# Kernel tuning notes

Measured on AMD Instinct MI355X. Metric: run time of the kernel, lower is better.

Reference implementation:

```python
import jax, jax.numpy as jnp
import numpy as np

N = 8192      # number of WSI patches
DIN = 1024    # input patch-feature dim (dim_in)
DH = 256      # dim_hidden
K = 6         # topk
SCALE = DH ** -0.5

def leaky(x):
    return jax.nn.leaky_relu(x, 0.01)

def setup_inputs() -> dict:
    key = jax.random.key(0)
    ks = jax.random.split(key, 8)
    def w(k, shape, fan_in):
        return jax.random.normal(k, shape, jnp.float32) / np.sqrt(fan_in).astype(np.float32)
    return {
        "x_path": jax.random.normal(ks[0], (N, DIN), jnp.float32),
        "fc1_W": w(ks[1], (DIN, DH), DIN), "fc1_b": jnp.zeros((DH,), jnp.float32),
        "Wh": w(ks[2], (DH, DH), DH), "bh": jnp.zeros((DH,), jnp.float32),
        "Wt": w(ks[3], (DH, DH), DH), "bt": jnp.zeros((DH,), jnp.float32),
        "W1": w(ks[4], (DH, DH), DH), "b1": jnp.zeros((DH,), jnp.float32),
        "W2": w(ks[5], (DH, DH), DH), "b2": jnp.zeros((DH,), jnp.float32),
        "Ag1": w(ks[6], (DH, DH // 2), DH), "bg1": jnp.zeros((DH // 2,), jnp.float32),
        "Ag2": w(ks[7], (DH // 2, 1), DH // 2), "bg2": jnp.zeros((1,), jnp.float32),
    }

def reference(x_path, fc1_W, fc1_b, Wh, bh, Wt, bt, W1, b1, W2, b2, Ag1, bg1, Ag2, bg2):
    # _fc1: Linear(1024->256) + LeakyReLU, then add global mean ("*0.5" mixing)
    x = leaky(x_path @ fc1_W + fc1_b)[None]                 # (1,N,DH)
    x = (x + x.mean(axis=1, keepdims=True)) * 0.5
    e_h = x @ Wh + bh                                        # (1,N,DH)
    e_t = x @ Wt + bt                                        # (1,N,DH)
    # dense attention logits, then top-k neighbor selection
    attn_logit = (e_h * SCALE) @ jnp.swapaxes(e_t, -1, -2)   # (1,N,N)
    topk_w, topk_i = jax.lax.top_k(attn_logit, K)            # (1,N,K)
    p = jax.nn.softmax(topk_w, axis=2)                       # (1,N,K)
    Nb_h = e_t[0][topk_i[0]][None]                           # gather: (1,N,K,DH)
    # message construction
    eh_r = p[..., None] * Nb_h + (1.0 - p)[..., None] * e_h[:, :, None, :]
    gate = jnp.tanh(e_h[:, :, None, :] + eh_r)               # (1,N,K,DH)
    # faithful to torch.einsum('ijkl,ijkm->ijk', Nb_h, gate):
    # l and m are independent -> separable double sum
    ka_w = Nb_h.sum(-1) * gate.sum(-1)                       # (1,N,K)
    ka_p = jax.nn.softmax(ka_w, axis=2)
    e_Nh = jnp.einsum('ink,inkd->ind', ka_p, Nb_h)           # (1,N,DH)
    # message MLPs (dropout in eval mode = identity)
    e_msg = leaky((e_h + e_Nh) @ W1 + b1) + leaky((e_h * e_Nh) @ W2 + b2)
    # GlobalAttention readout: gate_nn = Linear(256,128)+LeakyReLU+Linear(128,1)
    x2 = e_msg[0]                                            # (N,DH)
    g = leaky(x2 @ Ag1 + bg1) @ Ag2 + bg2                    # (N,1)
    g = jax.nn.softmax(g, axis=0)
    e_g = (g * x2).sum(axis=0, keepdims=True)                # (1,DH)
    return e_msg, e_g
```

## Files before the change

### kernel.cpp

```cpp
#include <hip/hip_runtime.h>


typedef __attribute__((ext_vector_type(8))) short short8;
typedef __attribute__((ext_vector_type(4))) short short4v;
typedef __attribute__((ext_vector_type(4))) float f32x4;

__device__ inline float bf2f(unsigned short b) {
    unsigned u = ((unsigned)b) << 16;
    return __builtin_bit_cast(float, u);
}
__device__ inline unsigned short f2bf(float f) {
    unsigned u = __builtin_bit_cast(unsigned, f);
    unsigned r = u + 0x7fffu + ((u >> 16) & 1u);
    return (unsigned short)(r >> 16);
}
__device__ inline f32x4 mfma16(short8 a, short8 b, f32x4 c) {
    return __builtin_amdgcn_mfma_f32_16x16x32_bf16(a, b, c, 0, 0, 0);
}

__device__ inline void gload_lds16(const unsigned short* g, unsigned short* l) {
    __builtin_amdgcn_global_load_lds(
        (const __attribute__((address_space(1))) void*)g,
        (__attribute__((address_space(3))) void*)l, 16, 0, 0);
}

__device__ inline void split8(const f32x4 v0, const f32x4 v1,
                              short8& hi, short8& md, short8& lo) {
    #pragma unroll
    for (int e = 0; e < 8; e++) {
        float a = (e < 4) ? v0[e] : v1[e - 4];
        unsigned ua = __builtin_bit_cast(unsigned, a);
        float h = __builtin_bit_cast(float, ua & 0xFFFF0000u);
        float r1 = a - h;
        unsigned u1 = __builtin_bit_cast(unsigned, r1);
        float m = __builtin_bit_cast(float, u1 & 0xFFFF0000u);
        float r2 = r1 - m;
        unsigned u2 = __builtin_bit_cast(unsigned, r2);
        hi[e] = (short)(ua >> 16);
        md[e] = (short)(u1 >> 16);
        lo[e] = (short)(u2 >> 16);
    }
}

__launch_bounds__(256)
__global__ void tsplit3(const float* __restrict__ W, unsigned short* __restrict__ out,
                        int K, int N, int PS) {
    __shared__ float T[32][33];
    const int t = threadIdx.x;
    const int n0 = blockIdx.x * 32, k0 = blockIdx.y * 32;
    {
        const int r = t >> 3, c = (t & 7) * 4;
        f32x4 v = *(const f32x4*)&W[(size_t)(k0 + r) * N + n0 + c];
        #pragma unroll
        for (int e = 0; e < 4; e++) T[r][c + e] = v[e];
    }
    __syncthreads();
    const int nr = t >> 3, kc = (t & 7) * 4;
    short4v h4, m4, l4;
    #pragma unroll
    for (int e = 0; e < 4; e++) {
        float a = T[kc + e][nr];
        unsigned short h = f2bf(a);
        float r1 = a - bf2f(h);
        unsigned short m = f2bf(r1);
        float r2 = r1 - bf2f(m);
        h4[e] = (short)h; m4[e] = (short)m; l4[e] = (short)f2bf(r2);
    }
    const size_t o = (size_t)(n0 + nr) * K + k0 + kc;
    *(short4v*)&out[o] = h4;
    *(short4v*)&out[(size_t)PS + o] = m4;
    *(short4v*)&out[(size_t)2 * PS + o] = l4;
}

template <int ASPLIT, int ACT, int ACCUM>
__launch_bounds__(256)
__global__ void gemmM(const void* __restrict__ Av,
                      const unsigned short* __restrict__ Bt,
                      const float* __restrict__ bias, float* __restrict__ C,
                      int N, int K, int BPS) {
    constexpr int APL = ASPLIT ? 3 : 1;
    constexpr int BPL = ASPLIT ? 3 : 2;
    __shared__ __align__(16) unsigned short LA[2][APL * 2048];
    __shared__ __align__(16) unsigned short LB[2][BPL * 2048];
    const int t = threadIdx.x;
    const int r0 = blockIdx.y * 64, c0 = blockIdx.x * 64;
    const int lid = t & 63, w = t >> 6, g = lid >> 4, m16 = lid & 15;
    const int wm = w >> 1, wn = w & 1;

    f32x4 acc[2][2];
    #pragma unroll
    for (int mf = 0; mf < 2; mf++)
        #pragma unroll
        for (int nf = 0; nf < 2; nf++) acc[mf][nf] = {0.0f, 0.0f, 0.0f, 0.0f};

    const int KT = K >> 5;
    const size_t aoff = (size_t)(r0 + (t >> 2)) * K + (t & 3) * 8;
    const size_t boff = (size_t)(c0 + (t >> 2)) * K + (t & 3) * 8;

    {
        #pragma unroll
        for (int p = 0; p < BPL; p++)
            gload_lds16(&Bt[(size_t)p * BPS + boff], &LB[0][p * 2048 + 8 * t]);
        if (ASPLIT) {
            const float* A = (const float*)Av;
            f32x4 v0 = *(const f32x4*)&A[aoff];
            f32x4 v1 = *(const f32x4*)&A[aoff + 4];
            short8 hi, md, lo;
            split8(v0, v1, hi, md, lo);
            *(short8*)&LA[0][8 * t] = hi;
            *(short8*)&LA[0][2048 + 8 * t] = md;
            *(short8*)&LA[0][4096 + 8 * t] = lo;
        } else {
            const unsigned short* A16 = (const unsigned short*)Av;
            gload_lds16(&A16[aoff], &LA[0][8 * t]);
        }
    }
    __syncthreads();

    for (int kt = 0; kt < KT; kt++) {
        const int cur = kt & 1, nxt = cur ^ 1;
        const bool hn = (kt + 1) < KT;
        f32x4 v0, v1;
        if (hn) {
            const size_t ko = (size_t)(kt + 1) * 32;
            #pragma unroll
            for (int p = 0; p < BPL; p++)
                gload_lds16(&Bt[(size_t)p * BPS + boff + ko],
                            &LB[nxt][p * 2048 + 8 * t]);
            if (ASPLIT) {
                const float* A = (const float*)Av;
                v0 = *(const f32x4*)&A[aoff + ko];
                v1 = *(const f32x4*)&A[aoff + ko + 4];
            } else {
                const unsigned short* A16 = (const unsigned short*)Av;
                gload_lds16(&A16[aoff + ko], &LA[nxt][8 * t]);
            }
        }
        short8 af[2][APL], bf[2][BPL];
        #pragma unroll
        for (int mf = 0; mf < 2; mf++) {
            const int row = wm * 32 + mf * 16 + m16;
            #pragma unroll
            for (int p = 0; p < APL; p++)
                af[mf][p] = *(const short8*)&LA[cur][p * 2048 + row * 32 + g * 8];
        }
        #pragma unroll
        for (int nf = 0; nf < 2; nf++) {
            const int col = wn * 32 + nf * 16 + m16;
            #pragma unroll
            for (int p = 0; p < BPL; p++)
                bf[nf][p] = *(const short8*)&LB[cur][p * 2048 + col * 32 + g * 8];
        }
        #pragma unroll
        for (int mf = 0; mf < 2; mf++)
            #pragma unroll
            for (int nf = 0; nf < 2; nf++) {
                if (ASPLIT) {
                    acc[mf][nf] = mfma16(af[mf][0], bf[nf][0], acc[mf][nf]);
                    acc[mf][nf] = mfma16(af[mf][0], bf[nf][1], acc[mf][nf]);
                    acc[mf][nf] = mfma16(af[mf][1], bf[nf][0], acc[mf][nf]);
                    acc[mf][nf] = mfma16(af[mf][0], bf[nf][2], acc[mf][nf]);
                    acc[mf][nf] = mfma16(af[mf][1], bf[nf][1], acc[mf][nf]);
                    acc[mf][nf] = mfma16(af[mf][2], bf[nf][0], acc[mf][nf]);
                } else {
                    acc[mf][nf] = mfma16(af[mf][0], bf[nf][0], acc[mf][nf]);
                    acc[mf][nf] = mfma16(af[mf][0], bf[nf][1], acc[mf][nf]);
                }
            }
        if (hn && ASPLIT) {
            short8 hi, md, lo;
            split8(v0, v1, hi, md, lo);
            *(short8*)&LA[nxt][8 * t] = hi;
            *(short8*)&LA[nxt][2048 + 8 * t] = md;
            *(short8*)&LA[nxt][4096 + 8 * t] = lo;
        }
        __syncthreads();
    }

    #pragma unroll
    for (int nf = 0; nf < 2; nf++) {
        const int col = c0 + wn * 32 + nf * 16 + m16;
        const float bv = bias[col];
        #pragma unroll
        for (int mf = 0; mf < 2; mf++) {
            #pragma unroll
            for (int r = 0; r < 4; r++) {
                const int row = r0 + wm * 32 + mf * 16 + g * 4 + r;
                float v = acc[mf][nf][r] + bv;
                if (ACT == 1) v = v > 0.0f ? v : 0.01f * v;
                size_t idx = (size_t)row * N + col;
                if (ACCUM) v += C[idx];
                C[idx] = v;
            }
        }
    }
}

__global__ void colsum_k(const float* __restrict__ x, float* __restrict__ out) {
    int d = threadIdx.x, b = blockIdx.x;
    float s = 0.0f;
    int i0 = b * 128;
    for (int i = 0; i < 128; i++) s += x[(size_t)(i0 + i) * 256 + d];
    out[b * 256 + d] = s;
}
__global__ void meanred_k(const float* __restrict__ p, float* __restrict__ mean) {
    int d = threadIdx.x;
    float s = 0.0f;
    for (int b = 0; b < 64; b++) s += p[b * 256 + d];
    mean[d] = s * (1.0f / 8192.0f);
}
__global__ void finalize_x(float* __restrict__ x, const float* __restrict__ mean) {
    size_t idx = (size_t)blockIdx.x * blockDim.x + threadIdx.x;
    f32x4 v = *(f32x4*)&x[idx * 4];
    int d4 = (int)((idx * 4) & 255);
    f32x4 m = *(const f32x4*)&mean[d4];
    #pragma unroll
    for (int e = 0; e < 4; e++) v[e] = (v[e] + m[e]) * 0.5f;
    *(f32x4*)&x[idx * 4] = v;
}
__launch_bounds__(256)
__global__ void prep_k(const float* __restrict__ eh, const float* __restrict__ et,
                       unsigned short* __restrict__ eh16,
                       unsigned short* __restrict__ et16,
                       float* __restrict__ rowsum) {
    const int b = blockIdx.x;
    if (b < 2048) {
        size_t idx = (size_t)b * 256 + threadIdx.x;
        f32x4 v = *(const f32x4*)&eh[idx * 4];
        short4v h;
        #pragma unroll
        for (int e = 0; e < 4; e++) h[e] = (short)f2bf(v[e]);
        *(short4v*)&eh16[idx * 4] = h;
    } else {
        const int w = threadIdx.x >> 6, l = threadIdx.x & 63;
        const int i = (b - 2048) * 4 + w;
        f32x4 v = *(const f32x4*)&et[(size_t)i * 256 + l * 4];
        short4v h;
        #pragma unroll
        for (int e = 0; e < 4; e++) h[e] = (short)f2bf(v[e]);
        *(short4v*)&et16[(size_t)i * 256 + l * 4] = h;
        float s = v[0] + v[1] + v[2] + v[3];
        #pragma unroll
        for (int st = 1; st < 64; st <<= 1) s += __shfl_xor(s, st);
        if (l == 0) rowsum[i] = s;
    }
}

__device__ inline float packkey(float v, unsigned col) {
    unsigned u = (__builtin_bit_cast(unsigned, v) & 0xFFFFF800u) | col;
    return __builtin_bit_cast(float, u);
}
template<int NK>
__device__ inline void insf(float (&tk)[NK], float key) {
    #pragma unroll
    for (int k = 0; k < NK - 1; k++)
        tk[k] = __builtin_amdgcn_fmed3f(key, tk[k + 1], tk[k]);
    tk[NK - 1] = fmaxf(tk[NK - 1], key);
}

__launch_bounds__(512)
__global__ void screen2(const unsigned short* __restrict__ eh16,
                        const unsigned short* __restrict__ et16,
                        int* __restrict__ candi) {
    __shared__ __align__(16) unsigned short Bs[2][2][8192];
    __shared__ float mbuf[8][2][16][8];
    const int t = threadIdx.x;
    const int cs = blockIdx.x;
    const int r0 = blockIdx.y * 128;
    const int w = t >> 6, lid = t & 63, lg = lid >> 4, m16 = lid & 15;
    const int rs = w >> 1, ch = w & 1;

    short8 bfr[2][8];
    #pragma unroll
    for (int s = 0; s < 2; s++)
        #pragma unroll
        for (int ks = 0; ks < 8; ks++)
            bfr[s][ks] = *(const short8*)
                &eh16[(size_t)(r0 + rs * 32 + s * 16 + m16) * 256 + ks * 32 + lg * 8];

    float tk0[6], tk1[6];
    #pragma unroll
    for (int q = 0; q < 6; q++) { tk0[q] = -3.0e38f; tk1[q] = -3.0e38f; }

    int scol[2], goff[2], ldsl[2];
    #pragma unroll
    for (int c = 0; c < 2; c++) {
        int L = (w * 2 + c) * 64 + lid;
        int col = L >> 5, gs = L & 31;
        int gorig = (gs & 24) | ((gs ^ col) & 7);
        scol[c] = col; goff[c] = gorig * 8; ldsl[c] = L * 8;
    }

    #pragma unroll
    for (int tt = 0; tt < 2; tt++) {
        const int j0 = cs * 2048 + tt * 32;
        #pragma unroll
        for (int c = 0; c < 2; c++)
            gload_lds16(&et16[(size_t)(j0 + scol[c]) * 256 + goff[c]],
                        &Bs[0][tt][ldsl[c]]);
    }
    __syncthreads();

    const int swz = m16 & 7;
    const int cbase = (ch * 16 + m16) * 32;
    for (int gi = 0; gi < 32; gi++) {
        const int cur = gi & 1;
        if (gi + 1 < 32) {
            #pragma unroll
            for (int tt = 0; tt < 2; tt++) {
                const int j1 = cs * 2048 + ((gi + 1) * 2 + tt) * 32;
                #pragma unroll
                for (int c = 0; c < 2; c++)
                    gload_lds16(&et16[(size_t)(j1 + scol[c]) * 256 + goff[c]],
                                &Bs[cur ^ 1][tt][ldsl[c]]);
            }
        }
        #pragma unroll
        for (int tt = 0; tt < 2; tt++) {
            const int tile = gi * 2 + tt;
            const unsigned short* bst = Bs[cur][tt];
            f32x4 a0 = {0.0f, 0.0f, 0.0f, 0.0f}, a1 = a0;
            #pragma unroll
            for (int ks = 0; ks < 8; ks++) {
                const int gq = ks * 4 + lg;
                short8 e = *(const short8*)&bst[(cbase + (gq ^ swz)) * 8];
                a0 = mfma16(e, bfr[0][ks], a0);
                a1 = mfma16(e, bfr[1][ks], a1);
            }
            const unsigned cb = (unsigned)(tile * 32 + ch * 16 + lg * 4);
            #pragma unroll
            for (int r = 0; r < 4; r++) {
                insf<6>(tk0, packkey(a0[r], cb + (unsigned)r));
                insf<6>(tk1, packkey(a1[r], cb + (unsigned)r));
            }
        }
        __syncthreads();
    }

    #pragma unroll
    for (int s = 0; s < 2; s++) {
        float tk8[8];
        tk8[0] = -3.0e38f; tk8[1] = -3.0e38f;
        #pragma unroll
        for (int q = 0; q < 6; q++) tk8[q + 2] = s ? tk1[q] : tk0[q];
        #pragma unroll
        for (int step = 16; step <= 32; step <<= 1) {
            float ok[8];
            #pragma unroll
            for (int q = 0; q < 8; q++) ok[q] = __shfl_xor(tk8[q], step);
            #pragma unroll
            for (int q = 0; q < 8; q++) insf<8>(tk8, ok[q]);
        }
        if (lg == 0) {
            #pragma unroll
            for (int q = 0; q < 8; q++) mbuf[rs * 2 + s][ch][m16][q] = tk8[q];
        }
    }
    __syncthreads();

    if (t < 128) {
        float tk8[8];
        #pragma unroll
        for (int q = 0; q < 8; q++) tk8[q] = mbuf[t >> 4][0][t & 15][q];
        #pragma unroll
        for (int q = 0; q < 8; q++) insf<8>(tk8, mbuf[t >> 4][1][t & 15][q]);
        const int row = r0 + t;
        #pragma unroll
        for (int q = 0; q < 8; q++)
            candi[(size_t)row * 32 + cs * 8 + q] =
                cs * 2048 + (int)(__builtin_bit_cast(unsigned, tk8[q]) & 0x7FFu);
    }
}

__launch_bounds__(256)
__global__ void stageD(const float* __restrict__ eh, const float* __restrict__ et,
                       const float* __restrict__ rowsum,
                       const int* __restrict__ candi,
                       unsigned short* __restrict__ m1, unsigned short* __restrict__ m2) {
    const int w = threadIdx.x >> 6, l = threadIdx.x & 63;
    const int i = blockIdx.x * 4 + w;
    const int c_own = l & 31;

    const int jown = candi[(size_t)i * 32 + c_own] & 8191;

    const int q = l & 7, g8 = l >> 3;
    const float* er = &eh[(size_t)i * 256];
    double vres[4];
    #pragma unroll
    for (int p = 0; p < 4; p++) {
        const int cc = p * 8 + g8;
        const int jc = __shfl(jown, cc);
        const float* tr = &et[(size_t)jc * 256];
        double a = 0.0;
        #pragma unroll
        for (int tt = 0; tt < 8; tt++) {
            const int o = (tt * 8 + q) * 4;
            f32x4 av = *(const f32x4*)&er[o];
            f32x4 bv = *(const f32x4*)&tr[o];
            a += (double)av[0] * bv[0] + (double)av[1] * bv[1] +
                 (double)av[2] * bv[2] + (double)av[3] * bv[3];
        }
        a += __shfl_xor(a, 1);
        a += __shfl_xor(a, 2);
        a += __shfl_xor(a, 4);
        vres[p] = a * 0.0625;
    }
    const int src = (c_own & 7) * 8;
    double t0 = __shfl(vres[0], src), t1 = __shfl(vres[1], src);
    double t2 = __shfl(vres[2], src), t3 = __shfl(vres[3], src);
    const int ps = c_own >> 3;
    double v = ps == 0 ? t0 : ps == 1 ? t1 : ps == 2 ? t2 : t3;

    unsigned long long kb = __builtin_bit_cast(unsigned long long, v);
    double key = __builtin_bit_cast(double, (kb & ~31ULL) | (unsigned long long)c_own);
    float wf[6]; int selc[6];
    #pragma unroll
    for (int s = 0; s < 6; s++) {
        double b = key;
        #pragma unroll
        for (int st = 1; st < 32; st <<= 1) {
            double ob = __shfl_xor(b, st);
            b = b > ob ? b : ob;
        }
        selc[s] = (int)(__builtin_bit_cast(unsigned long long, b) & 31ULL);
        wf[s] = (float)b;
        if (key == b) key = -1.0e300;
    }
    int selj[6];
    #pragma unroll
    for (int s = 0; s < 6; s++) selj[s] = __shfl(jown, selc[s]);

    float sp[6];
    {
        float mx = wf[0];
        #pragma unroll
        for (int s = 1; s < 6; s++) mx = fmaxf(mx, wf[s]);
        float se = 0.0f, e6[6];
        #pragma unroll
        for (int s = 0; s < 6; s++) { e6[s] = expf(wf[s] - mx); se += e6[s]; }
        #pragma unroll
        for (int s = 0; s < 6; s++) sp[s] = e6[s] / se;
    }

    f32x4 eh4 = *(const f32x4*)&eh[(size_t)i * 256 + l * 4];
    f32x4 nb[6];
    #pragma unroll
    for (int k = 0; k < 6; k++)
        nb[k] = *(const f32x4*)&et[(size_t)selj[k] * 256 + l * 4];

    float pgs[6], pns[6];
    #pragma unroll
    for (int k = 0; k < 6; k++) {
        const float pk = sp[k];
        float pg = 0.0f;
        #pragma unroll
        for (int e = 0; e < 4; e++) {
            float ehd = eh4[e], nbd = nb[k][e];
            float ehr = pk * nbd + (1.0f - pk) * ehd;
            pg += tanhf(ehd + ehr);
        }
        #pragma unroll
        for (int st = 1; st < 64; st <<= 1) pg += __shfl_xor(pg, st);
        pgs[k] = pg;
        pns[k] = rowsum[selj[k]];
    }

    float skp[6];
    {
        float ka[6], mx = -3.0e38f, se = 0.0f;
        #pragma unroll
        for (int k = 0; k < 6; k++) { ka[k] = pns[k] * pgs[k]; mx = fmaxf(mx, ka[k]); }
        #pragma unroll
        for (int k = 0; k < 6; k++) { ka[k] = expf(ka[k] - mx); se += ka[k]; }
        #pragma unroll
        for (int k = 0; k < 6; k++) skp[k] = ka[k] / se;
    }

    f32x4 enh = {0.0f, 0.0f, 0.0f, 0.0f};
    #pragma unroll
    for (int k = 0; k < 6; k++) {
        const float kp = skp[k];
        #pragma unroll
        for (int e = 0; e < 4; e++) enh[e] += kp * nb[k][e];
    }
    short4v h1, h2;
    #pragma unroll
    for (int e = 0; e < 4; e++) {
        h1[e] = (short)f2bf(eh4[e] + enh[e]);
        h2[e] = (short)f2bf(eh4[e] * enh[e]);
    }
    *(short4v*)&m1[(size_t)i * 256 + l * 4] = h1;
    *(short4v*)&m2[(size_t)i * 256 + l * 4] = h2;
}

__launch_bounds__(256)
__global__ void gate2_k(const float* __restrict__ g1, const float* __restrict__ Ag2,
                        const float* __restrict__ bg2, float* __restrict__ glog) {
    const int i = blockIdx.x * 256 + threadIdx.x;
    float s = 0.0f;
    #pragma unroll 4
    for (int h = 0; h < 128; h++) s += g1[(size_t)i * 128 + h] * Ag2[h];
    glog[i] = s + bg2[0];
}

__launch_bounds__(1024)
__global__ void softmax_g(const float* __restrict__ glog, float* __restrict__ gexp,
                          float* __restrict__ scal) {
    const int t = threadIdx.x;
    __shared__ float red[1024];
    float v[8];
    float m = -3.0e38f;
    #pragma unroll
    for (int c = 0; c < 8; c++) { v[c] = glog[t + c * 1024]; m = fmaxf(m, v[c]); }
    red[t] = m; __syncthreads();
    for (int st = 512; st > 0; st >>= 1) {
        if (t < st) red[t] = fmaxf(red[t], red[t + st]);
        __syncthreads();
    }
    float gm = red[0]; __syncthreads();
    float s = 0.0f;
    #pragma unroll
    for (int c = 0; c < 8; c++) {
        float e = expf(v[c] - gm);
        gexp[t + c * 1024] = e;
        s += e;
    }
    red[t] = s; __syncthreads();
    for (int st = 512; st > 0; st >>= 1) {
        if (t < st) red[t] += red[t + st];
        __syncthreads();
    }
    if (t == 0) scal[0] = 1.0f / red[0];
}

__launch_bounds__(256)
__global__ void wsum_k(const float* __restrict__ emsg, const float* __restrict__ gexp,
                       float* __restrict__ egp) {
    const int b = blockIdx.x, d = threadIdx.x;
    float s = 0.0f;
    const int i0 = b * 128;
    for (int i = 0; i < 128; i++) s += gexp[i0 + i] * emsg[(size_t)(i0 + i) * 256 + d];
    egp[b * 256 + d] = s;
}
__global__ void egfinal_f(const float* __restrict__ egp, const float* __restrict__ scal,
                          float* __restrict__ out) {
    const int d = threadIdx.x;
    float s = 0.0f;
    for (int b = 0; b < 64; b++) s += egp[b * 256 + d];
    out[d] = s * scal[0];
}

__global__ void wsbad_k(float* __restrict__ out) { out[3] = 9000.0f; }

extern "C" void kernel_launch(void* const* d_in, const int* in_sizes, int n_in,
                              void* d_out, int out_size, void* d_ws, size_t ws_size,
                              hipStream_t stream) {
    (void)in_sizes; (void)n_in; (void)out_size;
    const float* x_path = (const float*)d_in[0];
    const float* fc1_W  = (const float*)d_in[1];
    const float* fc1_b  = (const float*)d_in[2];
    const float* Wh     = (const float*)d_in[3];
    const float* bh     = (const float*)d_in[4];
    const float* Wt     = (const float*)d_in[5];
    const float* bt     = (const float*)d_in[6];
    const float* W1     = (const float*)d_in[7];
    const float* b1     = (const float*)d_in[8];
    const float* W2     = (const float*)d_in[9];
    const float* b2     = (const float*)d_in[10];
    const float* Ag1    = (const float*)d_in[11];
    const float* bg1    = (const float*)d_in[12];
    const float* Ag2    = (const float*)d_in[13];
    const float* bg2    = (const float*)d_in[14];
    float* out_f = (float*)d_out;

    const size_t WS_NEEDED = 26412048;
    if (ws_size < WS_NEEDED) {
        hipLaunchKernelGGL(wsbad_k, dim3(1), dim3(1), 0, stream, out_f);
        return;
    }

    char* ws = (char*)d_ws;
    float* x     = (float*)(ws + 0);
    unsigned short* eh16 = (unsigned short*)(ws + 0);
    unsigned short* et16 = (unsigned short*)(ws + 4194304);
    unsigned short* m1b  = (unsigned short*)(ws + 0);
    unsigned short* m2b  = (unsigned short*)(ws + 4194304);
    float* g1    = (float*)(ws + 0);
    float* eh    = (float*)(ws + 8388608);
    float* emsg  = out_f;
    float* et    = (float*)(ws + 16777216);
    int*   candi = (int*)  (ws + 25165824);
    float* rowsum= (float*)(ws + 26214400);
    float* meanp = (float*)(ws + 26214400);
    float* meanv = (float*)(ws + 26279936);
    float* glog  = (float*)(ws + 26280960);
    float* gexp  = (float*)(ws + 26313728);
    float* egp   = (float*)(ws + 26346496);
    float* scal  = (float*)(ws + 26412032);

    unsigned short* Fp = (unsigned short*)(ws + 16777216);
    unsigned short* WHp = (unsigned short*)(ws + 25165824);
    unsigned short* WTp = (unsigned short*)(ws + 25559040);
    unsigned short* P1 = (unsigned short*)(ws + 16777216);
    unsigned short* P2 = (unsigned short*)(ws + 17170432);
    unsigned short* Gp = (unsigned short*)(ws + 25165824);

    dim3 gg(4, 128);
    hipLaunchKernelGGL(tsplit3, dim3(8, 32), dim3(256), 0, stream,
                       fc1_W, Fp, 1024, 256, 262144);
    hipLaunchKernelGGL((gemmM<1, 1, 0>), gg, dim3(256), 0, stream,
                       (const void*)x_path, Fp, fc1_b, x, 256, 1024, 262144);
    hipLaunchKernelGGL(colsum_k, dim3(64), dim3(256), 0, stream, x, meanp);
    hipLaunchKernelGGL(meanred_k, dim3(1), dim3(256), 0, stream, meanp, meanv);
    hipLaunchKernelGGL(finalize_x, dim3(2048), dim3(256), 0, stream, x, meanv);
    hipLaunchKernelGGL(tsplit3, dim3(8, 8), dim3(256), 0, stream,
                       Wh, WHp, 256, 256, 65536);
    hipLaunchKernelGGL(tsplit3, dim3(8, 8), dim3(256), 0, stream,
                       Wt, WTp, 256, 256, 65536);
    hipLaunchKernelGGL((gemmM<1, 0, 0>), gg, dim3(256), 0, stream,
                       (const void*)x, WHp, bh, eh, 256, 256, 65536);
    hipLaunchKernelGGL((gemmM<1, 0, 0>), gg, dim3(256), 0, stream,
                       (const void*)x, WTp, bt, et, 256, 256, 65536);
    hipLaunchKernelGGL(prep_k, dim3(4096), dim3(256), 0, stream,
                       eh, et, eh16, et16, rowsum);
    hipLaunchKernelGGL(screen2, dim3(4, 64), dim3(512), 0, stream, eh16, et16, candi);
    hipLaunchKernelGGL(stageD, dim3(2048), dim3(256), 0, stream, eh, et, rowsum,
                       candi, m1b, m2b);
    hipLaunchKernelGGL(tsplit3, dim3(8, 8), dim3(256), 0, stream,
                       W1, P1, 256, 256, 65536);
    hipLaunchKernelGGL(tsplit3, dim3(8, 8), dim3(256), 0, stream,
                       W2, P2, 256, 256, 65536);
    hipLaunchKernelGGL((gemmM<0, 1, 0>), gg, dim3(256), 0, stream,
                       (const void*)m1b, P1, b1, emsg, 256, 256, 65536);
    hipLaunchKernelGGL((gemmM<0, 1, 1>), gg, dim3(256), 0, stream,
                       (const void*)m2b, P2, b2, emsg, 256, 256, 65536);
    hipLaunchKernelGGL(tsplit3, dim3(4, 8), dim3(256), 0, stream,
                       Ag1, Gp, 256, 128, 32768);
    hipLaunchKernelGGL((gemmM<1, 1, 0>), dim3(2, 128), dim3(256), 0, stream,
                       (const void*)emsg, Gp, bg1, g1, 128, 256, 32768);
    hipLaunchKernelGGL(gate2_k, dim3(32), dim3(256), 0, stream, g1, Ag2, bg2, glog);
    hipLaunchKernelGGL(softmax_g, dim3(1), dim3(1024), 0, stream, glog, gexp, scal);
    hipLaunchKernelGGL(wsum_k, dim3(64), dim3(256), 0, stream, emsg, gexp, egp);
    hipLaunchKernelGGL(egfinal_f, dim3(1), dim3(256), 0, stream, egp, scal, out_f + 2097152);
}
```

Baseline: 328.2 us.

## Fuse eh/et GEMMs, fold mean into bias, merge message MLP GEMMs

Replaces the finalize_x pass and the two separate eh/et GEMMs with one dual-output GEMM. It loads and splits x once, scales it by 0.5 inline, and folds the global-mean term into precomputed biases (bias + 0.5*mean@W). The two message-MLP GEMMs become one kernel that computes both products and writes leaky(a)+leaky(b), with no read-modify-write of emsg. Weight-split launches are also paired into single grids. This cuts launches and extra passes over global memory, but the mean is now folded in fp32 outside the split-bf16 path, which may change rounding slightly.

Result: faster. 312.0 us (-4.9%).

```diff
diff --git a/kernel.cpp b/kernel.cpp
--- a/kernel.cpp
+++ b/kernel.cpp
@@ -41,13 +41,28 @@
         lo[e] = (short)(u2 >> 16);
     }
 }
-
-__launch_bounds__(256)
-__global__ void tsplit3(const float* __restrict__ W, unsigned short* __restrict__ out,
-                        int K, int N, int PS) {
+__device__ inline void split4(f32x4 v, short4v& hi, short4v& md, short4v& lo) {
+    #pragma unroll
+    for (int e = 0; e < 4; e++) {
+        float a = v[e];
+        unsigned ua = __builtin_bit_cast(unsigned, a);
+        float h = __builtin_bit_cast(float, ua & 0xFFFF0000u);
+        float r1 = a - h;
+        unsigned u1 = __builtin_bit_cast(unsigned, r1);
+        float m = __builtin_bit_cast(float, u1 & 0xFFFF0000u);
+        float r2 = r1 - m;
+        unsigned u2 = __builtin_bit_cast(unsigned, r2);
+        hi[e] = (short)(ua >> 16);
+        md[e] = (short)(u1 >> 16);
+        lo[e] = (short)(u2 >> 16);
+    }
+}
+
+__device__ inline void tsplit_body(const float* __restrict__ W,
+                                   unsigned short* __restrict__ out,
+                                   int K, int N, int PS, int bx, int by, int t) {
     __shared__ float T[32][33];
-    const int t = threadIdx.x;
-    const int n0 = blockIdx.x * 32, k0 = blockIdx.y * 32;
+    const int n0 = bx * 32, k0 = by * 32;
     {
         const int r = t >> 3, c = (t & 7) * 4;
         f32x4 v = *(const f32x4*)&W[(size_t)(k0 + r) * N + n0 + c];
@@ -70,6 +85,18 @@
     *(short4v*)&out[o] = h4;
     *(short4v*)&out[(size_t)PS + o] = m4;
     *(short4v*)&out[(size_t)2 * PS + o] = l4;
+}
+__launch_bounds__(256)
+__global__ void tsplit3(const float* __restrict__ W, unsigned short* __restrict__ out,
+                        int K, int N, int PS) {
+    tsplit_body(W, out, K, N, PS, blockIdx.x, blockIdx.y, threadIdx.x);
+}
+__launch_bounds__(256)
+__global__ void tsplit3p(const float* __restrict__ Wa, const float* __restrict__ Wb,
+                         unsigned short* __restrict__ oa, unsigned short* __restrict__ ob,
+                         int K, int N, int PS) {
+    tsplit_body(blockIdx.z ? Wb : Wa, blockIdx.z ? ob : oa,
+                K, N, PS, blockIdx.x, blockIdx.y, threadIdx.x);
 }
 
 template <int ASPLIT, int ACT, int ACCUM>
@@ -196,6 +223,222 @@
     }
 }
 
+__launch_bounds__(512)
+__global__ void gemmD(const float* __restrict__ A,
+                      const unsigned short* __restrict__ BH,
+                      const unsigned short* __restrict__ BT,
+                      const float* __restrict__ biasH, const float* __restrict__ biasT,
+                      float* __restrict__ CH, float* __restrict__ CT, int BPS) {
+    __shared__ __align__(16) unsigned short LA[2][3 * 2048];
+    __shared__ __align__(16) unsigned short LB[2][6 * 2048];
+    const int t = threadIdx.x;
+    const int r0 = blockIdx.y * 64, c0 = blockIdx.x * 64;
+    const int lid = t & 63, w = t >> 6, g = lid >> 4, m16 = lid & 15;
+    const int mat = w >> 2, wsub = w & 3, wm = wsub >> 1, wn = wsub & 1;
+    const int K = 256;
+
+    f32x4 acc[2][2];
+    #pragma unroll
+    for (int mf = 0; mf < 2; mf++)
+        #pragma unroll
+        for (int nf = 0; nf < 2; nf++) acc[mf][nf] = {0.0f, 0.0f, 0.0f, 0.0f};
+
+    const int arow = t >> 3, akq = (t & 7) * 4;
+    const size_t aoff = (size_t)(r0 + arow) * K + akq;
+    const int aldst = arow * 32 + akq;
+    int bmp[3], bdst[3];
+    size_t bsrc[3];
+    #pragma unroll
+    for (int s = 0; s < 3; s++) {
+        int L = t + s * 512;
+        int mp = L >> 8;
+        bmp[s] = mp;
+        bdst[s] = mp * 2048 + (L & 255) * 8;
+        int mm = mp >= 3, pl = mp - 3 * mm;
+        const unsigned short* base = mm ? BT : BH;
+        bsrc[s] = (size_t)(base - BH) + (size_t)pl * BPS +
+                  (size_t)(c0 + ((L >> 2) & 63)) * K + (L & 3) * 8;
+    }
+
+    {
+        #pragma unroll
+        for (int s = 0; s < 3; s++)
+            gload_lds16(&BH[bsrc[s]], &LB[0][bdst[s]]);
+        f32x4 v = *(const f32x4*)&A[aoff];
+        #pragma unroll
+        for (int e = 0; e < 4; e++) v[e] *= 0.5f;
+        short4v hi, md, lo;
+        split4(v, hi, md, lo);
+        *(short4v*)&LA[0][aldst] = hi;
+        *(short4v*)&LA[0][2048 + aldst] = md;
+        *(short4v*)&LA[0][4096 + aldst] = lo;
+    }
+    __syncthreads();
+
+    for (int kt = 0; kt < 8; kt++) {
+        const int cur = kt & 1, nxt = cur ^ 1;
+        const bool hn = (kt + 1) < 8;
+        f32x4 v;
+        if (hn) {
+            const size_t ko = (size_t)(kt + 1) * 32;
+            #pragma unroll
+            for (int s = 0; s < 3; s++)
+                gload_lds16(&BH[bsrc[s] + ko], &LB[nxt][bdst[s]]);
+            v = *(const f32x4*)&A[aoff + ko];
+            #pragma unroll
+            for (int e = 0; e < 4; e++) v[e] *= 0.5f;
+        }
+        short8 af[2][3], bf[2][3];
+        #pragma unroll
+        for (int mf = 0; mf < 2; mf++) {
+            const int row = wm * 32 + mf * 16 + m16;
+            #pragma unroll
+            for (int p = 0; p < 3; p++)
+                af[mf][p] = *(const short8*)&LA[cur][p * 2048 + row * 32 + g * 8];
+        }
+        #pragma unroll
+        for (int nf = 0; nf < 2; nf++) {
+            const int col = wn * 32 + nf * 16 + m16;
+            #pragma unroll
+            for (int p = 0; p < 3; p++)
+                bf[nf][p] = *(const short8*)
+                    &LB[cur][(mat * 3 + p) * 2048 + col * 32 + g * 8];
+        }
+        #pragma unroll
+        for (int mf = 0; mf < 2; mf++)
+            #pragma unroll
+            for (int nf = 0; nf < 2; nf++) {
+                acc[mf][nf] = mfma16(af[mf][0], bf[nf][0], acc[mf][nf]);
+                acc[mf][nf] = mfma16(af[mf][0], bf[nf][1], acc[mf][nf]);
+                acc[mf][nf] = mfma16(af[mf][1], bf[nf][0], acc[mf][nf]);
+                acc[mf][nf] = mfma16(af[mf][0], bf[nf][2], acc[mf][nf]);
+                acc[mf][nf] = mfma16(af[mf][1], bf[nf][1], acc[mf][nf]);
+                acc[mf][nf] = mfma16(af[mf][2], bf[nf][0], acc[mf][nf]);
+            }
+        if (hn) {
+            short4v hi, md, lo;
+            split4(v, hi, md, lo);
+            *(short4v*)&LA[nxt][aldst] = hi;
+            *(short4v*)&LA[nxt][2048 + aldst] = md;
+            *(short4v*)&LA[nxt][4096 + aldst] = lo;
+        }
+        __syncthreads();
+    }
+
+    float* C = mat ? CT : CH;
+    const float* bias = mat ? biasT : biasH;
+    #pragma unroll
+    for (int nf = 0; nf < 2; nf++) {
+        const int col = c0 + wn * 32 + nf * 16 + m16;
+        const float bv = bias[col];
+        #pragma unroll
+        for (int mf = 0; mf < 2; mf++) {
+            #pragma unroll
+            for (int r = 0; r < 4; r++) {
+                const int row = r0 + wm * 32 + mf * 16 + g * 4 + r;
+                C[(size_t)row * 256 + col] = acc[mf][nf][r] + bv;
+            }
+        }
+    }
+}
+
+__launch_bounds__(256)
+__global__ void gemmE(const unsigned short* __restrict__ A1,
+                      const unsigned short* __restrict__ A2,
+                      const unsigned short* __restrict__ P1,
+                      const unsigned short* __restrict__ P2,
+                      const float* __restrict__ b1, const float* __restrict__ b2,
+                      float* __restrict__ C, int BPS) {
+    __shared__ __align__(16) unsigned short LA[2][2 * 2048];
+    __shared__ __align__(16) unsigned short LB[2][4 * 2048];
+    const int t = threadIdx.x;
+    const int r0 = blockIdx.y * 64, c0 = blockIdx.x * 64;
+    const int lid = t & 63, w = t >> 6, g = lid >> 4, m16 = lid & 15;
+    const int wm = w >> 1, wn = w & 1;
+    const int K = 256;
+
+    f32x4 acc[2][2][2];
+    #pragma unroll
+    for (int m = 0; m < 2; m++)
+        #pragma unroll
+        for (int mf = 0; mf < 2; mf++)
+            #pragma unroll
+            for (int nf = 0; nf < 2; nf++) acc[m][mf][nf] = {0.0f, 0.0f, 0.0f, 0.0f};
+
+    const size_t aoff = (size_t)(r0 + (t >> 2)) * K + (t & 3) * 8;
+    const size_t boff = (size_t)(c0 + (t >> 2)) * K + (t & 3) * 8;
+
+    {
+        gload_lds16(&A1[aoff], &LA[0][8 * t]);
+        gload_lds16(&A2[aoff], &LA[0][2048 + 8 * t]);
+        gload_lds16(&P1[boff], &LB[0][8 * t]);
+        gload_lds16(&P1[(size_t)BPS + boff], &LB[0][2048 + 8 * t]);
+        gload_lds16(&P2[boff], &LB[0][4096 + 8 * t]);
+        gload_lds16(&P2[(size_t)BPS + boff], &LB[0][6144 + 8 * t]);
+    }
+    __syncthreads();
+
+    for (int kt = 0; kt < 8; kt++) {
+        const int cur = kt & 1, nxt = cur ^ 1;
+        const bool hn = (kt + 1) < 8;
+        if (hn) {
+            const size_t ko = (size_t)(kt + 1) * 32;
+            gload_lds16(&A1[aoff + ko], &LA[nxt][8 * t]);
+            gload_lds16(&A2[aoff + ko], &LA[nxt][2048 + 8 * t]);
+            gload_lds16(&P1[boff + ko], &LB[nxt][8 * t]);
+            gload_lds16(&P1[(size_t)BPS + boff + ko], &LB[nxt][2048 + 8 * t]);
+            gload_lds16(&P2[boff + ko], &LB[nxt][4096 + 8 * t]);
+            gload_lds16(&P2[(size_t)BPS + boff + ko], &LB[nxt][6144 + 8 * t]);
+        }
+        short8 af[2][2], bf[2][2][2];
+        #pragma unroll
+        for (int m = 0; m < 2; m++)
+            #pragma unroll
+            for (int mf = 0; mf < 2; mf++) {
+                const int row = wm * 32 + mf * 16 + m16;
+                af[m][mf] = *(const short8*)&LA[cur][m * 2048 + row * 32 + g * 8];
+            }
+        #pragma unroll
+        for (int m = 0; m < 2; m++)
+            #pragma unroll
+            for (int nf = 0; nf < 2; nf++) {
+                const int col = wn * 32 + nf * 16 + m16;
+                #pragma unroll
+                for (int p = 0; p < 2; p++)
+                    bf[m][nf][p] = *(const short8*)
+                        &LB[cur][(m * 2 + p) * 2048 + col * 32 + g * 8];
+            }
+        #pragma unroll
+        for (int m = 0; m < 2; m++)
+            #pragma unroll
+            for (int mf = 0; mf < 2; mf++)
+                #pragma unroll
+                for (int nf = 0; nf < 2; nf++) {
+                    acc[m][mf][nf] = mfma16(af[m][mf], bf[m][nf][0], acc[m][mf][nf]);
+                    acc[m][mf][nf] = mfma16(af[m][mf], bf[m][nf][1], acc[m][mf][nf]);
+                }
+        __syncthreads();
+    }
+
+    #pragma unroll
+    for (int nf = 0; nf < 2; nf++) {
+        const int col = c0 + wn * 32 + nf * 16 + m16;
+        const float bv1 = b1[col], bv2 = b2[col];
+        #pragma unroll
+        for (int mf = 0; mf < 2; mf++) {
+            #pragma unroll
+            for (int r = 0; r < 4; r++) {
+                const int row = r0 + wm * 32 + mf * 16 + g * 4 + r;
+                float v1 = acc[0][mf][nf][r] + bv1;
+                v1 = v1 > 0.0f ? v1 : 0.01f * v1;
+                float v2 = acc[1][mf][nf][r] + bv2;
+                v2 = v2 > 0.0f ? v2 : 0.01f * v2;
+                C[(size_t)row * 256 + col] = v1 + v2;
+            }
+        }
+    }
+}
+
 __global__ void colsum_k(const float* __restrict__ x, float* __restrict__ out) {
     int d = threadIdx.x, b = blockIdx.x;
     float s = 0.0f;
@@ -209,14 +452,18 @@
     for (int b = 0; b < 64; b++) s += p[b * 256 + d];
     mean[d] = s * (1.0f / 8192.0f);
 }
-__global__ void finalize_x(float* __restrict__ x, const float* __restrict__ mean) {
-    size_t idx = (size_t)blockIdx.x * blockDim.x + threadIdx.x;
-    f32x4 v = *(f32x4*)&x[idx * 4];
-    int d4 = (int)((idx * 4) & 255);
-    f32x4 m = *(const f32x4*)&mean[d4];
-    #pragma unroll
-    for (int e = 0; e < 4; e++) v[e] = (v[e] + m[e]) * 0.5f;
-    *(f32x4*)&x[idx * 4] = v;
+__launch_bounds__(256)
+__global__ void mwv_k(const float* __restrict__ mean,
+                      const float* __restrict__ Wh, const float* __restrict__ bh,
+                      const float* __restrict__ Wt, const float* __restrict__ bt,
+                      float* __restrict__ biasH, float* __restrict__ biasT) {
+    const int n = threadIdx.x;
+    const float* W = blockIdx.x ? Wt : Wh;
+    const float* bb = blockIdx.x ? bt : bh;
+    float* o = blockIdx.x ? biasT : biasH;
+    float s = 0.0f;
+    for (int d = 0; d < 256; d++) s += mean[d] * W[d * 256 + n];
+    o[n] = bb[n] + 0.5f * s;
 }
 __launch_bounds__(256)
 __global__ void prep_k(const float* __restrict__ eh, const float* __restrict__ et,
@@ -592,6 +839,8 @@
     int*   candi = (int*)  (ws + 25165824);
     float* rowsum= (float*)(ws + 26214400);
     float* meanp = (float*)(ws + 26214400);
+    float* biasH = (float*)(ws + 26247168);
+    float* biasT = (float*)(ws + 26248192);
     float* meanv = (float*)(ws + 26279936);
     float* glog  = (float*)(ws + 26280960);
     float* gexp  = (float*)(ws + 26313728);
@@ -612,28 +861,21 @@
                        (const void*)x_path, Fp, fc1_b, x, 256, 1024, 262144);
     hipLaunchKernelGGL(colsum_k, dim3(64), dim3(256), 0, stream, x, meanp);
     hipLaunchKernelGGL(meanred_k, dim3(1), dim3(256), 0, stream, meanp, meanv);
-    hipLaunchKernelGGL(finalize_x, dim3(2048), dim3(256), 0, stream, x, meanv);
-    hipLaunchKernelGGL(tsplit3, dim3(8, 8), dim3(256), 0, stream,
-                       Wh, WHp, 256, 256, 65536);
-    hipLaunchKernelGGL(tsplit3, dim3(8, 8), dim3(256), 0, stream,
-                       Wt, WTp, 256, 256, 65536);
-    hipLaunchKernelGGL((gemmM<1, 0, 0>), gg, dim3(256), 0, stream,
-                       (const void*)x, WHp, bh, eh, 256, 256, 65536);
-    hipLaunchKernelGGL((gemmM<1, 0, 0>), gg, dim3(256), 0, stream,
-                       (const void*)x, WTp, bt, et, 256, 256, 65536);
+    hipLaunchKernelGGL(tsplit3p, dim3(8, 8, 2), dim3(256), 0, stream,
+                       Wh, Wt, WHp, WTp, 256, 256, 65536);
+    hipLaunchKernelGGL(mwv_k, dim3(2), dim3(256), 0, stream,
+                       meanv, Wh, bh, Wt, bt, biasH, biasT);
+    hipLaunchKernelGGL(gemmD, gg, dim3(512), 0, stream,
+                       x, WHp, WTp, biasH, biasT, eh, et, 65536);
     hipLaunchKernelGGL(prep_k, dim3(4096), dim3(256), 0, stream,
                        eh, et, eh16, et16, rowsum);
     hipLaunchKernelGGL(screen2, dim3(4, 64), dim3(512), 0, stream, eh16, et16, candi);
     hipLaunchKernelGGL(stageD, dim3(2048), dim3(256), 0, stream, eh, et, rowsum,
                        candi, m1b, m2b);
-    hipLaunchKernelGGL(tsplit3, dim3(8, 8), dim3(256), 0, stream,
-                       W1, P1, 256, 256, 65536);
-    hipLaunchKernelGGL(tsplit3, dim3(8, 8), dim3(256), 0, stream,
-                       W2, P2, 256, 256, 65536);
-    hipLaunchKernelGGL((gemmM<0, 1, 0>), gg, dim3(256), 0, stream,
-                       (const void*)m1b, P1, b1, emsg, 256, 256, 65536);
-    hipLaunchKernelGGL((gemmM<0, 1, 1>), gg, dim3(256), 0, stream,
-                       (const void*)m2b, P2, b2, emsg, 256, 256, 65536);
+    hipLaunchKernelGGL(tsplit3p, dim3(8, 8, 2), dim3(256), 0, stream,
+                       W1, W2, P1, P2, 256, 256, 65536);
+    hipLaunchKernelGGL(gemmE, gg, dim3(256), 0, stream,
+                       m1b, m2b, P1, P2, b1, b2, emsg, 65536);
     hipLaunchKernelGGL(tsplit3, dim3(4, 8), dim3(256), 0, stream,
                        Ag1, Gp, 256, 128, 32768);
     hipLaunchKernelGGL((gemmM<1, 1, 0>), dim3(2, 128), dim3(256), 0, stream,
```
